# Kernel optimization log

Hardware: AMD Instinct MI355X
Metric: run time of the kernel (lower is better)

The kernel has to match this reference:

```python
import jax, jax.numpy as jnp
import numpy as np

ATOM_DIM, HID, N_LAYERS, N_HEADS, PF_DIM = 34, 256, 2, 8, 1024
B, NA, NP = 32, 512, 1024


def setup_inputs() -> dict:
    key = jax.random.key(0)
    ks = iter(jax.random.split(key, 32))
    def rn(shape, s=0.02):
        return jax.random.normal(next(ks), shape, dtype=jnp.float32) * s
    L = N_LAYERS
    z = lambda *s: jnp.zeros(s, jnp.float32)
    return {
        "trg": jax.random.normal(next(ks), (B, NA, ATOM_DIM), dtype=jnp.float32),
        "src": jax.random.normal(next(ks), (B, NP, HID), dtype=jnp.float32),
        "ft_w": rn((HID, ATOM_DIM)), "ft_b": z(HID),
        "ln_g": jnp.ones((L, HID), jnp.float32), "ln_b": z(L, HID),
        "sa_wq": rn((L, HID, HID)), "sa_bq": z(L, HID),
        "sa_wk": rn((L, HID, HID)), "sa_bk": z(L, HID),
        "sa_wv": rn((L, HID, HID)), "sa_bv": z(L, HID),
        "sa_wf": rn((L, HID, HID)), "sa_bf": z(L, HID),
        "ea_wq": rn((L, HID, HID)), "ea_bq": z(L, HID),
        "ea_wk": rn((L, HID, HID)), "ea_bk": z(L, HID),
        "ea_wv": rn((L, HID, HID)), "ea_bv": z(L, HID),
        "ea_wf": rn((L, HID, HID)), "ea_bf": z(L, HID),
        "pf_w1": rn((L, PF_DIM, HID)), "pf_b1": z(L, PF_DIM),
        "pf_w2": rn((L, HID, PF_DIM)), "pf_b2": z(L, HID),
        "fc1_w": rn((256, HID)), "fc1_b": z(256),
        "fc2_w": rn((2, 256)), "fc2_b": z(2),
    }


def _ln(x, g, b, eps=1e-5):
    m = jnp.mean(x, axis=-1, keepdims=True)
    v = jnp.mean(jnp.square(x - m), axis=-1, keepdims=True)
    return (x - m) * jax.lax.rsqrt(v + eps) * g + b


def _attn(xq, xkv, wq, bq, wk, bk, wv, bv, wf, bf):
    b_, lq, h = xq.shape
    d = h // N_HEADS
    q = (xq @ wq.T + bq).reshape(b_, lq, N_HEADS, d).transpose(0, 2, 1, 3)
    k = (xkv @ wk.T + bk).reshape(b_, -1, N_HEADS, d).transpose(0, 2, 1, 3)
    v = (xkv @ wv.T + bv).reshape(b_, -1, N_HEADS, d).transpose(0, 2, 1, 3)
    scale = jnp.sqrt(jnp.float32(d))  # TransformerCPI: sqrt(hid_dim // n_heads)
    a = jax.nn.softmax(jnp.einsum('bhqd,bhkd->bhqk', q, k) / scale, axis=-1)
    o = jnp.einsum('bhqk,bhkd->bhqd', a, v).transpose(0, 2, 1, 3).reshape(b_, lq, h)
    return o @ wf.T + bf


def reference(trg, src, ft_w, ft_b, ln_g, ln_b,
              sa_wq, sa_bq, sa_wk, sa_bk, sa_wv, sa_bv, sa_wf, sa_bf,
              ea_wq, ea_bq, ea_wk, ea_bk, ea_wv, ea_bv, ea_wf, ea_bf,
              pf_w1, pf_b1, pf_w2, pf_b2, fc1_w, fc1_b, fc2_w, fc2_b):
    x = trg @ ft_w.T + ft_b  # [B, NA, HID]
    for l in range(N_LAYERS):
        x = _ln(x + _attn(x, x, sa_wq[l], sa_bq[l], sa_wk[l], sa_bk[l],
                          sa_wv[l], sa_bv[l], sa_wf[l], sa_bf[l]), ln_g[l], ln_b[l])
        x = _ln(x + _attn(x, src, ea_wq[l], ea_bq[l], ea_wk[l], ea_bk[l],
                          ea_wv[l], ea_bv[l], ea_wf[l], ea_bf[l]), ln_g[l], ln_b[l])
        h = jax.nn.relu(x @ pf_w1[l].T + pf_b1[l]) @ pf_w2[l].T + pf_b2[l]
        x = _ln(x + h, ln_g[l], ln_b[l])
    # norm-weighted attention pooling (replaces the nested Python loops)
    w = jax.nn.softmax(jnp.linalg.norm(x, axis=2), axis=1)  # [B, NA]
    pooled = jnp.einsum('bn,bnh->bh', w, x)  # [B, HID]
    return jax.nn.relu(pooled @ fc1_w.T + fc1_b) @ fc2_w.T + fc2_b
```

## Files before the change

kernel.cpp:

```cpp
#include <hip/hip_runtime.h>
#include <hip/hip_bf16.h>
#include <math.h>

#define B_   32
#define NA   512
#define NP   1024
#define HID  256
#define NH   8
#define DH   32
#define PF   1024

typedef short bf16x8 __attribute__((ext_vector_type(8)));
typedef float f32x4  __attribute__((ext_vector_type(4)));
typedef float f32x16 __attribute__((ext_vector_type(16)));
typedef unsigned u32x4 __attribute__((ext_vector_type(4)));

#define ZERO16 {0.f,0.f,0.f,0.f,0.f,0.f,0.f,0.f,0.f,0.f,0.f,0.f,0.f,0.f,0.f,0.f}

static __device__ inline unsigned short f2bf(float f) {
    __hip_bfloat16 h = __float2bfloat16(f);
    unsigned short u;
    __builtin_memcpy(&u, &h, 2);
    return u;
}
static __device__ inline float bf2f(unsigned short u) {
    unsigned x = ((unsigned)u) << 16;
    return __uint_as_float(x);
}
static __device__ inline unsigned cvtpk(float lo, float hi) {
    return (unsigned)f2bf(lo) | ((unsigned)f2bf(hi) << 16);
}
static __device__ inline bf16x8 pack8(float4 a, float4 b) {
    bf16x8 r;
    r[0] = (short)f2bf(a.x); r[1] = (short)f2bf(a.y);
    r[2] = (short)f2bf(a.z); r[3] = (short)f2bf(a.w);
    r[4] = (short)f2bf(b.x); r[5] = (short)f2bf(b.y);
    r[6] = (short)f2bf(b.z); r[7] = (short)f2bf(b.w);
    return r;
}

__global__ __launch_bounds__(256) void ft_kernel(const float* __restrict__ trg,
    const float* __restrict__ w, const float* __restrict__ b,
    float* __restrict__ out, unsigned short* __restrict__ outb)
{
    __shared__ float Ws[256][35];
    int tid = threadIdx.x;
    for (int k = 0; k < 34; ++k) Ws[tid][k] = w[tid*34 + k];
    float bias = b[tid];
    __syncthreads();
    int m0 = blockIdx.x * 32;
    for (int r = 0; r < 32; ++r) {
        int m = m0 + r;
        const float* tr = trg + (size_t)m*34;
        float acc = bias;
        #pragma unroll
        for (int k = 0; k < 34; ++k) acc += tr[k] * Ws[tid][k];
        out [(size_t)m*HID + tid] = acc;
        outb[(size_t)m*HID + tid] = f2bf(acc);
    }
}

__global__ __launch_bounds__(256) void cvt_bf16(const float* __restrict__ in,
    unsigned short* __restrict__ outb, int n8)
{
    int i = blockIdx.x*256 + threadIdx.x;
    int stride = gridDim.x*256;
    for (; i < n8; i += stride) {
        float4 a = *(const float4*)(in + (size_t)i*8);
        float4 b = *(const float4*)(in + (size_t)i*8 + 4);
        *(bf16x8*)(outb + (size_t)i*8) = pack8(a, b);
    }
}

__global__ __launch_bounds__(256) void cvt_w(
    const float* __restrict__ s0, const float* __restrict__ s1,
    const float* __restrict__ s2, const float* __restrict__ s3,
    const float* __restrict__ s4, const float* __restrict__ s5,
    const float* __restrict__ s6, const float* __restrict__ s7,
    const float* __restrict__ s8, const float* __restrict__ s9,
    unsigned short* __restrict__ dst)
{
    const int z = blockIdx.z;
    const float* src;
    switch (z) {
        case 0: src = s0; break; case 1: src = s1; break;
        case 2: src = s2; break; case 3: src = s3; break;
        case 4: src = s4; break; case 5: src = s5; break;
        case 6: src = s6; break; case 7: src = s7; break;
        case 8: src = s8; break; default: src = s9; break;
    }
    const int n8 = (z < 8) ? 16384 : 65536;
    const size_t off = (z < 8) ? (size_t)z*131072 : (1048576u + (size_t)(z-8)*524288);
    unsigned short* o = dst + off;
    int i = blockIdx.x*256 + threadIdx.x;
    const int stride = gridDim.x*256;
    for (; i < n8; i += stride) {
        float4 a = *(const float4*)(src + (size_t)i*8);
        float4 b = *(const float4*)(src + (size_t)i*8 + 4);
        *(bf16x8*)(o + (size_t)i*8) = pack8(a, b);
    }
}

static __device__ inline void gemm_core(const unsigned short* __restrict__ Ab,
    const unsigned short* __restrict__ Wb, const float* __restrict__ bias,
    void* __restrict__ Cv, int M, int N, int K, int mode, int L, float oscale,
    int bx, int by)
{
    __shared__ __attribute__((aligned(16))) unsigned short As[128][72];
    __shared__ __attribute__((aligned(16))) unsigned short Bs[64][72];
    const int tid = threadIdx.x;
    const int wave = tid >> 6, lane = tid & 63, lq = lane & 15, g = lane >> 4;
    const int wr = wave >> 1, wc = wave & 1;
    const int m0 = by * 128, n0 = bx * 64;

    const int ar = tid >> 1, ac = (tid & 1) * 32;
    const int br = tid >> 2, bc = (tid & 3) * 16;

    f32x4 acc[4][2] = {};
    bf16x8 sa[4], sw[2];

    auto LOAD = [&](int kt) {
        const int k0 = kt * 64;
        const unsigned short* Ap = Ab + (size_t)(m0 + ar)*K + k0 + ac;
        #pragma unroll
        for (int i = 0; i < 4; ++i)
            sa[i] = *(const bf16x8*)(Ap + i*8);
        const unsigned short* Wp = Wb + (size_t)(n0 + br)*K + k0 + bc;
        #pragma unroll
        for (int i = 0; i < 2; ++i)
            sw[i] = *(const bf16x8*)(Wp + i*8);
    };
    auto STORE = [&]() {
        #pragma unroll
        for (int i = 0; i < 4; ++i) *(bf16x8*)&As[ar][ac + i*8] = sa[i];
        #pragma unroll
        for (int i = 0; i < 2; ++i) *(bf16x8*)&Bs[br][bc + i*8] = sw[i];
    };

    const int nk = K / 64;
    LOAD(0);
    for (int kt = 0; kt < nk; ++kt) {
        __syncthreads();
        STORE();
        __syncthreads();
        if (kt + 1 < nk) LOAD(kt + 1);
        #pragma unroll
        for (int ks = 0; ks < 2; ++ks) {
            bf16x8 bf0 = *(const bf16x8*)&Bs[wc*32 +  0 + lq][ks*32 + g*8];
            bf16x8 bf1 = *(const bf16x8*)&Bs[wc*32 + 16 + lq][ks*32 + g*8];
            #pragma unroll
            for (int i = 0; i < 4; ++i) {
                bf16x8 af = *(const bf16x8*)&As[wr*64 + i*16 + lq][ks*32 + g*8];
                acc[i][0] = __builtin_amdgcn_mfma_f32_16x16x32_bf16(af, bf0, acc[i][0], 0, 0, 0);
                acc[i][1] = __builtin_amdgcn_mfma_f32_16x16x32_bf16(af, bf1, acc[i][1], 0, 0, 0);
            }
        }
    }

    float bb[2];
    #pragma unroll
    for (int j = 0; j < 2; ++j) bb[j] = bias[n0 + wc*32 + j*16 + lq];

    #pragma unroll
    for (int i = 0; i < 4; ++i) {
        const int mb = m0 + wr*64 + i*16 + 4*g;
        #pragma unroll
        for (int j = 0; j < 2; ++j) {
            const int n = n0 + wc*32 + j*16 + lq;
            f32x4 v = acc[i][j];
            #pragma unroll
            for (int r = 0; r < 4; ++r) v[r] = (v[r] + bb[j]) * oscale;
            if (mode == 0) {
                float* Cf = (float*)Cv;
                #pragma unroll
                for (int r = 0; r < 4; ++r) Cf[(size_t)(mb + r)*N + n] = v[r];
            } else if (mode == 1) {
                unsigned short* Cb = (unsigned short*)Cv;
                #pragma unroll
                for (int r = 0; r < 4; ++r) Cb[(size_t)(mb + r)*N + n] = f2bf(v[r]);
            } else if (mode == 3) {
                unsigned short* Cb = (unsigned short*)Cv;
                #pragma unroll
                for (int r = 0; r < 4; ++r) Cb[(size_t)(mb + r)*N + n] = f2bf(fmaxf(v[r], 0.f));
            } else if (mode == 4) {
                unsigned short* Cb = (unsigned short*)Cv;
                const int bI = mb / L, kk = mb % L;
                const int hh = n >> 5, d = n & 31;
                const int t2 = kk >> 5, dc = d >> 4, hi2 = (d >> 3) & 1;
                unsigned short* base = Cb
                    + ((size_t)(((bI*NH + hh)*(L >> 5) + t2)*2 + dc))*512
                    + ((kk & 31) + 32*hi2)*8 + (d & 7);
                base[0]  = f2bf(v[0]); base[8]  = f2bf(v[1]);
                base[16] = f2bf(v[2]); base[24] = f2bf(v[3]);
            } else {
                unsigned short* Cb = (unsigned short*)Cv;
                const int bI = mb / L, kk = mb % L;
                const int hh = n >> 5, d = n & 31;
                const int t = kk >> 6, oct = (kk >> 3) & 7;
                const int c = oct >> 1, hiV = oct & 1;
                ushort4 pk;
                pk.x = f2bf(v[0]); pk.y = f2bf(v[1]); pk.z = f2bf(v[2]); pk.w = f2bf(v[3]);
                *(ushort4*)(Cb
                    + ((size_t)(((bI*NH + hh)*(L >> 6) + t)*4 + c))*512
                    + (d + 32*hiV)*8 + (kk & 7)) = pk;
            }
        }
    }
}

static __device__ inline void xcd_swz(int d, int nx, int nxy, int& bx, int& by)
{
    const int w = (d & 7) * (nxy >> 3) + (d >> 3);
    bx = w % nx; by = w / nx;
}

__global__ __launch_bounds__(256) void gemm_mfma(const unsigned short* __restrict__ A,
    const unsigned short* __restrict__ W, const float* __restrict__ bias,
    void* __restrict__ C, int M, int N, int K, int mode, int L)
{
    int bx, by;
    xcd_swz(blockIdx.y*gridDim.x + blockIdx.x, gridDim.x, gridDim.x*gridDim.y, bx, by);
    gemm_core(A, W, bias, C, M, N, K, mode, L, 1.f, bx, by);
}

__global__ __launch_bounds__(256) void qkv_mfma(const unsigned short* __restrict__ Aq,
    const unsigned short* __restrict__ Akv,
    const unsigned short* __restrict__ Wq, const float* __restrict__ bq,
    const unsigned short* __restrict__ Wk, const float* __restrict__ bk,
    const unsigned short* __restrict__ Wv, const float* __restrict__ bv,
    void* __restrict__ qo, void* __restrict__ ko, void* __restrict__ vo,
    int Mq, int Mkv, int L)
{
    const int z = blockIdx.z;
    const unsigned short* A = (z == 0) ? Aq : Akv;
    const unsigned short* W = (z == 0) ? Wq : ((z == 1) ? Wk : Wv);
    const float* bb = (z == 0) ? bq : ((z == 1) ? bk : bv);
    void* C = (z == 0) ? qo : ((z == 1) ? ko : vo);
    const int M = (z == 0) ? Mq : Mkv;
    const int mode = (z == 0) ? 1 : ((z == 1) ? 4 : 5);
    const float sc = (z == 0) ? 0.25504082364238727f : 1.f;
    int bx, by;
    xcd_swz(blockIdx.y*gridDim.x + blockIdx.x, gridDim.x, gridDim.x*gridDim.y, bx, by);
    if (by * 128 >= M) return;
    gemm_core(A, W, bb, C, M, HID, HID, mode, L, sc, bx, by);
}

__global__ __launch_bounds__(256) void attn_mfma(const unsigned short* __restrict__ Qb,
    const unsigned short* __restrict__ KF, const unsigned short* __restrict__ VF,
    unsigned short* __restrict__ O, int Lk)
{
    __shared__ float Ll[4][32];
    const int orig = blockIdx.x;
    const int sw = (orig & 7) * 128 + (orig >> 3);
    const int qt = sw & 3;
    const int h  = (sw >> 2) & 7;
    const int b  = sw >> 5;
    const int tid = threadIdx.x, w = tid >> 6, lane = tid & 63;
    const int q32 = lane & 31, hi = lane >> 5;

    const unsigned short* qp = Qb + ((size_t)(b*NA + qt*128 + w*32 + q32))*HID + h*DH + hi*8;
    bf16x8 qf0 = *(const bf16x8*)qp;
    bf16x8 qf1 = *(const bf16x8*)(qp + 16);

    const unsigned short* Kf = KF + (size_t)((b*NH + h)*(Lk >> 5)*2)*512 + lane*8;
    const unsigned short* Vf = VF + (size_t)((b*NH + h)*(Lk >> 6)*4)*512 + lane*8;

    f32x16 o_acc = ZERO16;
    float lacc = 0.f;

    bf16x8 kfA[4], kfB[4], vfT[4];
    auto LOADK = [&](int t, bf16x8* kd) {
        #pragma unroll
        for (int f = 0; f < 4; ++f)
            kd[f] = *(const bf16x8*)(Kf + (size_t)(t*4 + f)*512);
    };
    auto STEP = [&](const bf16x8* kf, int t) {
        #pragma unroll
        for (int c = 0; c < 4; ++c)
            vfT[c] = *(const bf16x8*)(Vf + (size_t)(t*4 + c)*512);
        f32x16 st0 = ZERO16, st1 = ZERO16;
        st0 = __builtin_amdgcn_mfma_f32_32x32x16_bf16(kf[0], qf0, st0, 0, 0, 0);
        st0 = __builtin_amdgcn_mfma_f32_32x32x16_bf16(kf[1], qf1, st0, 0, 0, 0);
        st1 = __builtin_amdgcn_mfma_f32_32x32x16_bf16(kf[2], qf0, st1, 0, 0, 0);
        st1 = __builtin_amdgcn_mfma_f32_32x32x16_bf16(kf[3], qf1, st1, 0, 0, 0);
        bf16x8 pa[4];
        float lp = 0.f;
        #pragma unroll
        for (int c = 0; c < 4; ++c) {
            const f32x16& s = (c < 2) ? st0 : st1;
            const int rb = (c & 1) * 8;
            float p0 = __builtin_amdgcn_exp2f(s[rb+0]);
            float p1 = __builtin_amdgcn_exp2f(s[rb+1]);
            float p2 = __builtin_amdgcn_exp2f(s[rb+2]);
            float p3 = __builtin_amdgcn_exp2f(s[rb+3]);
            float p4 = __builtin_amdgcn_exp2f(s[rb+4]);
            float p5 = __builtin_amdgcn_exp2f(s[rb+5]);
            float p6 = __builtin_amdgcn_exp2f(s[rb+6]);
            float p7 = __builtin_amdgcn_exp2f(s[rb+7]);
            lp += (p0+p1) + (p2+p3) + (p4+p5) + (p6+p7);
            unsigned A1 = cvtpk(p0, p1), A2 = cvtpk(p2, p3);
            unsigned B1 = cvtpk(p4, p5), B2 = cvtpk(p6, p7);
            auto r1 = __builtin_amdgcn_permlane32_swap(A1, B1, false, false);
            auto r2 = __builtin_amdgcn_permlane32_swap(A2, B2, false, false);
            u32x4 pw; pw[0] = r1[0]; pw[1] = r2[0]; pw[2] = r1[1]; pw[3] = r2[1];
            __builtin_memcpy(&pa[c], &pw, 16);
        }
        lacc += lp;
        #pragma unroll
        for (int c = 0; c < 4; ++c)
            o_acc = __builtin_amdgcn_mfma_f32_32x32x16_bf16(pa[c], vfT[c], o_acc, 0, 0, 0);
    };

    const int nt = Lk >> 6;
    LOADK(0, kfA);
    for (int t = 0; t < nt; t += 2) {
        LOADK(t + 1, kfB);
        STEP(kfA, t);
        if (t + 2 < nt) LOADK(t + 2, kfA);
        STEP(kfB, t + 1);
    }

    float lt = lacc + __shfl_xor(lacc, 32);
    float linv = 1.f / lt;
    if (hi == 0) Ll[w][q32] = linv;
    f32x4 li[4];
    #pragma unroll
    for (int jg = 0; jg < 4; ++jg) li[jg] = *(const f32x4*)&Ll[w][jg*8 + hi*4];

    unsigned short* Op = O + ((size_t)(b*NA + qt*128 + w*32))*HID + h*DH + q32;
    #pragma unroll
    for (int jg = 0; jg < 4; ++jg) {
        #pragma unroll
        for (int r2 = 0; r2 < 4; ++r2) {
            const int q = jg*8 + hi*4 + r2;
            Op[(size_t)q*HID] = f2bf(o_acc[jg*4 + r2] * li[jg][r2]);
        }
    }
}

__global__ __launch_bounds__(256) void add_ln(float* __restrict__ x,
    const unsigned short* __restrict__ t, const float* __restrict__ g,
    const float* __restrict__ bt, unsigned short* __restrict__ xb)
{
    const int row = blockIdx.x*4 + (threadIdx.x >> 6);
    const int lane = threadIdx.x & 63;
    const size_t base = (size_t)row*HID + lane*4;
    float4 v = *(const float4*)(x + base);
    ushort4 tu = *(const ushort4*)(t + base);
    v.x += bf2f(tu.x); v.y += bf2f(tu.y); v.z += bf2f(tu.z); v.w += bf2f(tu.w);
    float s = v.x + v.y + v.z + v.w;
    #pragma unroll
    for (int o = 32; o > 0; o >>= 1) s += __shfl_xor(s, o);
    float mean = s * (1.f/256.f);
    float4 d = {v.x - mean, v.y - mean, v.z - mean, v.w - mean};
    float q2 = d.x*d.x + d.y*d.y + d.z*d.z + d.w*d.w;
    #pragma unroll
    for (int o = 32; o > 0; o >>= 1) q2 += __shfl_xor(q2, o);
    float rs = rsqrtf(q2*(1.f/256.f) + 1e-5f);
    float4 gv = *(const float4*)(g + lane*4);
    float4 bv = *(const float4*)(bt + lane*4);
    float4 ov;
    ov.x = d.x*rs*gv.x + bv.x; ov.y = d.y*rs*gv.y + bv.y;
    ov.z = d.z*rs*gv.z + bv.z; ov.w = d.w*rs*gv.w + bv.w;
    *(float4*)(x + base) = ov;
    ushort4 pk;
    pk.x = f2bf(ov.x); pk.y = f2bf(ov.y); pk.z = f2bf(ov.z); pk.w = f2bf(ov.w);
    *(ushort4*)(xb + base) = pk;
}

__global__ __launch_bounds__(256) void norms_k(const float* __restrict__ x,
    float* __restrict__ nw)
{
    const int row = blockIdx.x*4 + (threadIdx.x >> 6);
    const int lane = threadIdx.x & 63;
    float4 v = *(const float4*)(x + (size_t)row*HID + lane*4);
    float s = v.x*v.x + v.y*v.y + v.z*v.z + v.w*v.w;
    #pragma unroll
    for (int o = 32; o > 0; o >>= 1) s += __shfl_xor(s, o);
    if (lane == 0) nw[row] = sqrtf(s);
}

__global__ __launch_bounds__(256) void pooled_k(const float* __restrict__ x,
    const float* __restrict__ nw, float* __restrict__ pooled)
{
    __shared__ float sw[NA];
    __shared__ float red[256];
    __shared__ float part[8][33];
    const int b = blockIdx.x, hc = blockIdx.y;
    const int tid = threadIdx.x;
    const float* nb = nw + (size_t)b*NA;
    float v0 = nb[tid], v1 = nb[tid + 256];
    red[tid] = fmaxf(v0, v1); __syncthreads();
    for (int s = 128; s > 0; s >>= 1) { if (tid < s) red[tid] = fmaxf(red[tid], red[tid+s]); __syncthreads(); }
    float mx = red[0]; __syncthreads();
    float e0 = __expf(v0 - mx), e1 = __expf(v1 - mx);
    sw[tid] = e0; sw[tid + 256] = e1;
    red[tid] = e0 + e1; __syncthreads();
    for (int s = 128; s > 0; s >>= 1) { if (tid < s) red[tid] += red[tid+s]; __syncthreads(); }
    float inv = 1.f / red[0];
    __syncthreads();
    const int ng = tid >> 5, col = tid & 31;
    const float* xp = x + (size_t)b*NA*HID + hc*32 + col;
    float acc = 0.f;
    for (int n = ng; n < NA; n += 8)
        acc += sw[n] * xp[(size_t)n*HID];
    part[ng][col] = acc;
    __syncthreads();
    if (tid < 32) {
        float s = 0.f;
        #pragma unroll
        for (int i = 0; i < 8; ++i) s += part[i][tid];
        pooled[(size_t)b*HID + hc*32 + tid] = s * inv;
    }
}

__global__ __launch_bounds__(256) void head_k(const float* __restrict__ pooled,
    const float* __restrict__ fc1w, const float* __restrict__ fc1b,
    const float* __restrict__ fc2w, const float* __restrict__ fc2b,
    float* __restrict__ out)
{
    __shared__ float p[HID];
    __shared__ float a1[HID];
    const int b = blockIdx.x, tid = threadIdx.x;
    p[tid] = pooled[(size_t)b*HID + tid];
    __syncthreads();
    float s1 = fc1b[tid];
    const float* w1 = fc1w + (size_t)tid*HID;
    for (int k2 = 0; k2 < HID; k2 += 4) {
        float4 w = *(const float4*)(w1 + k2);
        s1 += p[k2]*w.x + p[k2+1]*w.y + p[k2+2]*w.z + p[k2+3]*w.w;
    }
    a1[tid] = fmaxf(s1, 0.f);
    __syncthreads();
    if (tid < 2) {
        float s2 = fc2b[tid];
        const float* w2 = fc2w + (size_t)tid*HID;
        for (int k2 = 0; k2 < HID; ++k2) s2 += a1[k2] * w2[k2];
        out[b*2 + tid] = s2;
    }
}

extern "C" void kernel_launch(void* const* d_in, const int* in_sizes, int n_in,
                              void* d_out, int out_size, void* d_ws, size_t ws_size,
                              hipStream_t stream)
{
    const float* trg  = (const float*)d_in[0];
    const float* src  = (const float*)d_in[1];
    const float* ft_w = (const float*)d_in[2];
    const float* ft_b = (const float*)d_in[3];
    const float* ln_g = (const float*)d_in[4];
    const float* ln_b = (const float*)d_in[5];
    const float* sa_wq = (const float*)d_in[6];  const float* sa_bq = (const float*)d_in[7];
    const float* sa_wk = (const float*)d_in[8];  const float* sa_bk = (const float*)d_in[9];
    const float* sa_wv = (const float*)d_in[10]; const float* sa_bv = (const float*)d_in[11];
    const float* sa_wf = (const float*)d_in[12]; const float* sa_bf = (const float*)d_in[13];
    const float* ea_wq = (const float*)d_in[14]; const float* ea_bq = (const float*)d_in[15];
    const float* ea_wk = (const float*)d_in[16]; const float* ea_bk = (const float*)d_in[17];
    const float* ea_wv = (const float*)d_in[18]; const float* ea_bv = (const float*)d_in[19];
    const float* ea_wf = (const float*)d_in[20]; const float* ea_bf = (const float*)d_in[21];
    const float* pf_w1 = (const float*)d_in[22]; const float* pf_b1 = (const float*)d_in[23];
    const float* pf_w2 = (const float*)d_in[24]; const float* pf_b2 = (const float*)d_in[25];
    const float* fc1w  = (const float*)d_in[26]; const float* fc1b  = (const float*)d_in[27];
    const float* fc2w  = (const float*)d_in[28]; const float* fc2b  = (const float*)d_in[29];
    float* out = (float*)d_out;

    const size_t NTOK = (size_t)B_*NA;
    const size_t NSRC = (size_t)B_*NP;
    float* ws = (float*)d_ws;
    float* x  = ws;
    float* nw = x + NTOK*HID;
    float* pooled = nw + NTOK;
    unsigned short* ub   = (unsigned short*)(pooled + B_*HID);
    unsigned short* xb   = ub + NTOK*HID;
    unsigned short* tb   = xb + NTOK*HID;
    unsigned short* srcb = tb + NTOK*HID;
    unsigned short* qb   = srcb + NSRC*HID;
    unsigned short* kb   = qb + NTOK*HID;
    unsigned short* vTb  = kb + NSRC*HID;
    unsigned short* wb   = vTb + NSRC*HID;
    unsigned short* hb   = qb;

    unsigned short* saq_b = wb;
    unsigned short* sak_b = wb +  131072;
    unsigned short* sav_b = wb +  262144;
    unsigned short* saf_b = wb +  393216;
    unsigned short* eaq_b = wb +  524288;
    unsigned short* eak_b = wb +  655360;
    unsigned short* eav_b = wb +  786432;
    unsigned short* eaf_b = wb +  917504;
    unsigned short* pw1_b = wb + 1048576;
    unsigned short* pw2_b = wb + 1572864;

    const int M = (int)NTOK;
    dim3 blk(256);

    cvt_w<<<dim3(64, 1, 10), blk, 0, stream>>>(sa_wq, sa_wk, sa_wv, sa_wf,
        ea_wq, ea_wk, ea_wv, ea_wf, pf_w1, pf_w2, wb);
    ft_kernel<<<M/32, blk, 0, stream>>>(trg, ft_w, ft_b, x, xb);
    cvt_bf16<<<1024, blk, 0, stream>>>(src, srcb, (int)(NSRC*HID/8));

    for (int l = 0; l < 2; ++l) {
        const size_t wo = (size_t)l*HID*HID, bo = (size_t)l*HID;
        qkv_mfma<<<dim3(HID/64, M/128, 3), blk, 0, stream>>>(xb, xb,
            saq_b+wo, sa_bq+bo, sak_b+wo, sa_bk+bo, sav_b+wo, sa_bv+bo,
            qb, kb, vTb, M, M, NA);
        attn_mfma<<<dim3(1024), blk, 0, stream>>>(qb, kb, vTb, tb, NA);
        gemm_mfma<<<dim3(HID/64, M/128), blk, 0, stream>>>(tb, saf_b+wo, sa_bf+bo, ub, M, HID, HID, 1, 0);
        add_ln<<<M/4, blk, 0, stream>>>(x, ub, ln_g+bo, ln_b+bo, xb);
        qkv_mfma<<<dim3(HID/64, (int)NSRC/128, 3), blk, 0, stream>>>(xb, srcb,
            eaq_b+wo, ea_bq+bo, eak_b+wo, ea_bk+bo, eav_b+wo, ea_bv+bo,
            qb, kb, vTb, M, (int)NSRC, NP);
        attn_mfma<<<dim3(1024), blk, 0, stream>>>(qb, kb, vTb, tb, NP);
        gemm_mfma<<<dim3(HID/64, M/128), blk, 0, stream>>>(tb, eaf_b+wo, ea_bf+bo, ub, M, HID, HID, 1, 0);
        add_ln<<<M/4, blk, 0, stream>>>(x, ub, ln_g+bo, ln_b+bo, xb);
        gemm_mfma<<<dim3(PF/64, M/128), blk, 0, stream>>>(xb, pw1_b+(size_t)l*PF*HID, pf_b1+(size_t)l*PF, hb, M, PF, HID, 3, 0);
        gemm_mfma<<<dim3(HID/64, M/128), blk, 0, stream>>>(hb, pw2_b+(size_t)l*HID*PF, pf_b2+bo, ub, M, HID, PF, 1, 0);
        add_ln<<<M/4, blk, 0, stream>>>(x, ub, ln_g+bo, ln_b+bo, xb);
    }

    norms_k<<<M/4, blk, 0, stream>>>(x, nw);
    pooled_k<<<dim3(B_, 8), blk, 0, stream>>>(x, nw, pooled);
    head_k<<<B_, blk, 0, stream>>>(pooled, fc1w, fc1b, fc2w, fc2b, out);
}
```

Before: 444.3 us.

## Double-buffer GEMM tiles via direct global-to-LDS loads with XOR swizzle

Replaces the register-staged load/store of A and W tiles in the shared GEMM core with direct global_load_lds 16-byte transfers into double-buffered LDS tiles. It applies an XOR column swizzle in place of padding to avoid bank conflicts, and cuts the two barriers per k-step to one. The goal is to overlap the next tile's fetch with the current MFMA work and to free VGPRs. The single trailing barrier may not order the asynchronous LDS writes correctly without explicit vmcnt waits, and LDS use doubles.

```diff
diff --git a/kernel.cpp b/kernel.cpp
--- a/kernel.cpp
+++ b/kernel.cpp
@@ -37,6 +37,11 @@
     r[4] = (short)f2bf(b.x); r[5] = (short)f2bf(b.y);
     r[6] = (short)f2bf(b.z); r[7] = (short)f2bf(b.w);
     return r;
+}
+static __device__ inline void gload16(const unsigned short* g, unsigned short* l) {
+    __builtin_amdgcn_global_load_lds(
+        (const __attribute__((address_space(1))) void*)g,
+        (__attribute__((address_space(3))) void*)l, 16, 0, 0);
 }
 
 __global__ __launch_bounds__(256) void ft_kernel(const float* __restrict__ trg,
@@ -106,55 +111,56 @@
     void* __restrict__ Cv, int M, int N, int K, int mode, int L, float oscale,
     int bx, int by)
 {
-    __shared__ __attribute__((aligned(16))) unsigned short As[128][72];
-    __shared__ __attribute__((aligned(16))) unsigned short Bs[64][72];
+    __shared__ __attribute__((aligned(16))) unsigned short As[2][128*64];
+    __shared__ __attribute__((aligned(16))) unsigned short Ws[2][64*64];
     const int tid = threadIdx.x;
     const int wave = tid >> 6, lane = tid & 63, lq = lane & 15, g = lane >> 4;
     const int wr = wave >> 1, wc = wave & 1;
     const int m0 = by * 128, n0 = bx * 64;
 
-    const int ar = tid >> 1, ac = (tid & 1) * 32;
-    const int br = tid >> 2, bc = (tid & 3) * 16;
+    const int srow = lane >> 3;
+    const int scol = ((lane & 7) ^ ((lane >> 3) & 7)) * 8;
+    const int cswz = (lq & 7) * 8;
 
     f32x4 acc[4][2] = {};
-    bf16x8 sa[4], sw[2];
-
-    auto LOAD = [&](int kt) {
+
+    auto STAGE = [&](int kt, int buf) {
         const int k0 = kt * 64;
-        const unsigned short* Ap = Ab + (size_t)(m0 + ar)*K + k0 + ac;
-        #pragma unroll
-        for (int i = 0; i < 4; ++i)
-            sa[i] = *(const bf16x8*)(Ap + i*8);
-        const unsigned short* Wp = Wb + (size_t)(n0 + br)*K + k0 + bc;
-        #pragma unroll
-        for (int i = 0; i < 2; ++i)
-            sw[i] = *(const bf16x8*)(Wp + i*8);
+        #pragma unroll
+        for (int c = 0; c < 4; ++c) {
+            const int row = wave*32 + c*8;
+            gload16(Ab + (size_t)(m0 + row + srow)*K + k0 + scol,
+                    &As[buf][row*64]);
+        }
+        #pragma unroll
+        for (int c = 0; c < 2; ++c) {
+            const int row = wave*16 + c*8;
+            gload16(Wb + (size_t)(n0 + row + srow)*K + k0 + scol,
+                    &Ws[buf][row*64]);
+        }
     };
-    auto STORE = [&]() {
-        #pragma unroll
-        for (int i = 0; i < 4; ++i) *(bf16x8*)&As[ar][ac + i*8] = sa[i];
-        #pragma unroll
-        for (int i = 0; i < 2; ++i) *(bf16x8*)&Bs[br][bc + i*8] = sw[i];
-    };
 
     const int nk = K / 64;
-    LOAD(0);
+    STAGE(0, 0);
+    __syncthreads();
     for (int kt = 0; kt < nk; ++kt) {
-        __syncthreads();
-        STORE();
-        __syncthreads();
-        if (kt + 1 < nk) LOAD(kt + 1);
+        const int cur = kt & 1;
+        if (kt + 1 < nk) STAGE(kt + 1, cur ^ 1);
+        const unsigned short* Ac = &As[cur][0];
+        const unsigned short* Wc = &Ws[cur][0];
         #pragma unroll
         for (int ks = 0; ks < 2; ++ks) {
-            bf16x8 bf0 = *(const bf16x8*)&Bs[wc*32 +  0 + lq][ks*32 + g*8];
-            bf16x8 bf1 = *(const bf16x8*)&Bs[wc*32 + 16 + lq][ks*32 + g*8];
+            const int co = (ks*32 + g*8) ^ cswz;
+            bf16x8 bf0 = *(const bf16x8*)&Wc[(wc*32 +  0 + lq)*64 + co];
+            bf16x8 bf1 = *(const bf16x8*)&Wc[(wc*32 + 16 + lq)*64 + co];
             #pragma unroll
             for (int i = 0; i < 4; ++i) {
-                bf16x8 af = *(const bf16x8*)&As[wr*64 + i*16 + lq][ks*32 + g*8];
+                bf16x8 af = *(const bf16x8*)&Ac[(wr*64 + i*16 + lq)*64 + co];
                 acc[i][0] = __builtin_amdgcn_mfma_f32_16x16x32_bf16(af, bf0, acc[i][0], 0, 0, 0);
                 acc[i][1] = __builtin_amdgcn_mfma_f32_16x16x32_bf16(af, bf1, acc[i][1], 0, 0, 0);
             }
         }
+        __syncthreads();
     }
 
     float bb[2];
```

New measurement: 443.1 us. Within noise of the previous version (-0.3%).
